# Kernel tuning notes

Measured on AMD Instinct MI355X. Metric: run time of the kernel, lower is better.

## Reference

```python
import jax, jax.numpy as jnp
import numpy as np

N = 8192
IN_DIM = 128
HID = 32


def setup_inputs() -> dict:
    key = jax.random.key(0)
    ks = jax.random.split(key, 8)
    x = jax.random.normal(ks[0], (N, IN_DIM), dtype=jnp.float32)
    adj = jax.random.uniform(ks[1], (N, N), dtype=jnp.float32)
    # Linear params (torch nn.Linear: y = x @ W.T + b); store as [in, out] for einsum.
    def lin(k, fan_in, fan_out):
        bound = 1.0 / np.sqrt(fan_in)
        kw, kb = jax.random.split(k)
        W = jax.random.uniform(kw, (fan_in, fan_out), minval=-bound, maxval=bound, dtype=jnp.float32)
        b = jax.random.uniform(kb, (fan_out,), minval=-bound, maxval=bound, dtype=jnp.float32)
        return W, b
    W1, b1 = lin(ks[2], IN_DIM, HID)
    W2, b2 = lin(ks[3], HID, HID)
    W3, b3 = lin(ks[4], HID, 1)
    return {"x": x, "adj": adj, "W1": W1, "b1": b1, "W2": W2, "b2": b2, "W3": W3, "b3": b3}


def reference(x, adj, W1, b1, W2, b2, W3, b3):
    # a_hat = adj + I (self loops)
    n = adj.shape[0]
    a_hat = adj + jnp.eye(n, dtype=adj.dtype)
    degree = jnp.sum(a_hat, axis=1)
    d_inv_sqrt = jnp.clip(degree, 1.0, None) ** -0.5  # [N]
    # D^-1/2 A D^-1/2 as row/col scaling (same math as diag matmuls, no O(N^3) waste)
    a_norm = d_inv_sqrt[:, None] * a_hat * d_inv_sqrt[None, :]
    h = jax.nn.relu(a_norm @ (x @ W1 + b1))
    h = jax.nn.relu(a_norm @ (h @ W2 + b2))
    logits = (h @ W3 + b3).squeeze(-1)  # [N]
    return logits
```

## Files before the change

### kernel.cpp

```cpp
#include <hip/hip_runtime.h>
#include <math.h>

#define N 8192
#define IN_DIM 128
#define HID 32

#define RB 128
#define KT 64
#define SK 8
#define KCHUNK (N / SK)

__device__ __forceinline__ void fma4(float4& acc, float a, const float4& b) {
    acc.x = fmaf(a, b.x, acc.x);
    acc.y = fmaf(a, b.y, acc.y);
    acc.z = fmaf(a, b.z, acc.z);
    acc.w = fmaf(a, b.w, acc.w);
}

__global__ __launch_bounds__(256) void k_degree(const float* __restrict__ adj,
                                                float* __restrict__ dinv) {
    int row = blockIdx.x;
    const float4* rp = (const float4*)(adj + (size_t)row * N);
    int t = threadIdx.x;
    float s = 0.f;
#pragma unroll
    for (int i = 0; i < 8; ++i) {
        float4 v = rp[t + i * 256];
        s += v.x + v.y + v.z + v.w;
    }
    for (int off = 32; off > 0; off >>= 1) s += __shfl_down(s, off, 64);
    __shared__ float red[4];
    if ((t & 63) == 0) red[t >> 6] = s;
    __syncthreads();
    if (t == 0) {
        float deg = red[0] + red[1] + red[2] + red[3] + 1.0f;
        deg = fmaxf(deg, 1.0f);
        dinv[row] = 1.0f / sqrtf(deg);
    }
}

__global__ __launch_bounds__(256) void k_z1(const float* __restrict__ x,
                                            const float* __restrict__ W1,
                                            const float* __restrict__ b1,
                                            const float* __restrict__ dinv,
                                            float* __restrict__ Zs) {
    __shared__ float Ws[IN_DIM * HID];
    __shared__ float xs[8 * IN_DIM];
    int t = threadIdx.x;
    int row0 = blockIdx.x * 8;
#pragma unroll
    for (int i = 0; i < 4; ++i)
        *(float4*)&Ws[(i * 256 + t) * 4] = *(const float4*)&W1[(i * 256 + t) * 4];
    *(float4*)&xs[t * 4] = *(const float4*)&x[(size_t)row0 * IN_DIM + t * 4];
    __syncthreads();
    int r = t >> 5, c = t & 31;
    float acc = b1[c];
#pragma unroll 8
    for (int k = 0; k < IN_DIM; ++k) acc = fmaf(xs[r * IN_DIM + k], Ws[k * HID + c], acc);
    int row = row0 + r;
    Zs[(size_t)row * HID + c] = dinv[row] * acc;
}

__global__ __launch_bounds__(256) void k_z2(const float* __restrict__ Hin,
                                            const float* __restrict__ W2,
                                            const float* __restrict__ b2,
                                            const float* __restrict__ dinv,
                                            float* __restrict__ Zs) {
    __shared__ float Ws[HID * HID];
    __shared__ float hs[8 * HID];
    int t = threadIdx.x;
    int row0 = blockIdx.x * 8;
    *(float4*)&Ws[t * 4] = *(const float4*)&W2[t * 4];
    if (t < 64) *(float4*)&hs[t * 4] = *(const float4*)&Hin[(size_t)row0 * HID + t * 4];
    __syncthreads();
    int r = t >> 5, c = t & 31;
    float acc = b2[c];
#pragma unroll
    for (int k = 0; k < HID; ++k) acc = fmaf(hs[r * HID + k], Ws[k * HID + c], acc);
    int row = row0 + r;
    Zs[(size_t)row * HID + c] = dinv[row] * acc;
}

__global__ __launch_bounds__(256) void k_spmm(const float* __restrict__ adj,
                                              const float* __restrict__ Zs,
                                              float* __restrict__ P) {
    __shared__ float As[RB][KT + 4];
    __shared__ float Bs[KT][HID];
    int t = threadIdx.x;
    int r0 = blockIdx.x * RB;
    int k0 = blockIdx.y * KCHUNK;
    int cg = t & 3;
    int rp2 = (t >> 2) * 2;
    float4 acc00 = {0, 0, 0, 0}, acc01 = {0, 0, 0, 0};
    float4 acc10 = {0, 0, 0, 0}, acc11 = {0, 0, 0, 0};

    for (int kt = k0; kt < k0 + KCHUNK; kt += KT) {
#pragma unroll
        for (int i = 0; i < 8; ++i) {
            int f = i * 256 + t;
            int row = f >> 4;
            int kc = (f & 15) << 2;
            *(float4*)&As[row][kc] = *(const float4*)&adj[(size_t)(r0 + row) * N + kt + kc];
        }
#pragma unroll
        for (int i = 0; i < 2; ++i) {
            int f = i * 256 + t;
            ((float4*)&Bs[0][0])[f] = ((const float4*)(Zs + (size_t)kt * HID))[f];
        }
        __syncthreads();
#pragma unroll
        for (int kk = 0; kk < KT; kk += 4) {
            float a0[4], a1[4];
            *(float4*)a0 = *(const float4*)&As[rp2][kk];
            *(float4*)a1 = *(const float4*)&As[rp2 + 1][kk];
#pragma unroll
            for (int j = 0; j < 4; ++j) {
                float4 z0 = *(const float4*)&Bs[kk + j][cg * 8];
                float4 z1 = *(const float4*)&Bs[kk + j][cg * 8 + 4];
                fma4(acc00, a0[j], z0);
                fma4(acc01, a0[j], z1);
                fma4(acc10, a1[j], z0);
                fma4(acc11, a1[j], z1);
            }
        }
        __syncthreads();
    }

    float* p0 = P + (size_t)(r0 + rp2) * HID + cg * 8;
    float* p1 = p0 + HID;
    atomicAdd(p0 + 0, acc00.x); atomicAdd(p0 + 1, acc00.y);
    atomicAdd(p0 + 2, acc00.z); atomicAdd(p0 + 3, acc00.w);
    atomicAdd(p0 + 4, acc01.x); atomicAdd(p0 + 5, acc01.y);
    atomicAdd(p0 + 6, acc01.z); atomicAdd(p0 + 7, acc01.w);
    atomicAdd(p1 + 0, acc10.x); atomicAdd(p1 + 1, acc10.y);
    atomicAdd(p1 + 2, acc10.z); atomicAdd(p1 + 3, acc10.w);
    atomicAdd(p1 + 4, acc11.x); atomicAdd(p1 + 5, acc11.y);
    atomicAdd(p1 + 6, acc11.z); atomicAdd(p1 + 7, acc11.w);
}

__global__ __launch_bounds__(256) void k_fin(const float* __restrict__ P,
                                             const float* __restrict__ Zs,
                                             const float* __restrict__ dinv,
                                             float* __restrict__ H) {
    int idx = blockIdx.x * 256 + threadIdx.x;
    int row = idx >> 5;
    float v = dinv[row] * (P[idx] + Zs[idx]);
    H[idx] = fmaxf(v, 0.f);
}

__global__ __launch_bounds__(256) void k_out(const float* __restrict__ H,
                                             const float* __restrict__ W3,
                                             const float* __restrict__ b3,
                                             float* __restrict__ out) {
    int i = blockIdx.x * 256 + threadIdx.x;
    const float4* hr = (const float4*)(H + (size_t)i * HID);
    const float4* w = (const float4*)W3;
    float acc = b3[0];
#pragma unroll
    for (int kk = 0; kk < 8; ++kk) {
        float4 h = hr[kk], ww = w[kk];
        acc += h.x * ww.x + h.y * ww.y + h.z * ww.z + h.w * ww.w;
    }
    out[i] = acc;
}

extern "C" void kernel_launch(void* const* d_in, const int* in_sizes, int n_in,
                              void* d_out, int out_size, void* d_ws, size_t ws_size,
                              hipStream_t stream) {
    const float* x   = (const float*)d_in[0];
    const float* adj = (const float*)d_in[1];
    const float* W1  = (const float*)d_in[2];
    const float* b1  = (const float*)d_in[3];
    const float* W2  = (const float*)d_in[4];
    const float* b2  = (const float*)d_in[5];
    const float* W3  = (const float*)d_in[6];
    const float* b3  = (const float*)d_in[7];
    float* out = (float*)d_out;

    float* dinv = (float*)d_ws;
    float* Zs   = dinv + N;
    float* P    = Zs + (size_t)N * HID;
    float* H    = P + (size_t)N * HID;

    k_degree<<<N, 256, 0, stream>>>(adj, dinv);
    k_z1<<<N / 8, 256, 0, stream>>>(x, W1, b1, dinv, Zs);

    hipMemsetAsync(P, 0, (size_t)N * HID * sizeof(float), stream);
    k_spmm<<<dim3(N / RB, SK), 256, 0, stream>>>(adj, Zs, P);
    k_fin<<<N * HID / 256, 256, 0, stream>>>(P, Zs, dinv, H);

    k_z2<<<N / 8, 256, 0, stream>>>(H, W2, b2, dinv, Zs);

    hipMemsetAsync(P, 0, (size_t)N * HID * sizeof(float), stream);
    k_spmm<<<dim3(N / RB, SK), 256, 0, stream>>>(adj, Zs, P);
    k_fin<<<N * HID / 256, 256, 0, stream>>>(P, Zs, dinv, H);

    k_out<<<N / 256, 256, 0, stream>>>(H, W3, b3, out);
}
```

Baseline: 611.9 us.

## Convert adjacency to fp16 once and use fdot2 SpMM with fused epilogue

The degree kernel now also writes an fp16 copy of the adjacency matrix. Both aggregation passes then stream that half-size copy instead of fp32. The SpMM is restructured: Z is stored transposed in fp16 and double-buffered in shared memory, each wave handles 4 rows across the full K range, and the inner product uses packed fp16 dot2 instructions. Split-K atomics, the memset and the separate finalize kernel are replaced by an in-block reduction that fuses the dinv scaling, self-loop add and ReLU. This cuts adjacency traffic for the two passes at the cost of one extra fp16 write and reduced precision.

Result: slower. 1.117 ms (+82.5%).

```diff
diff --git a/kernel.cpp b/kernel.cpp
--- a/kernel.cpp
+++ b/kernel.cpp
@@ -5,27 +5,46 @@
 #define IN_DIM 128
 #define HID 32
 
-#define RB 128
-#define KT 64
-#define SK 8
-#define KCHUNK (N / SK)
-
-__device__ __forceinline__ void fma4(float4& acc, float a, const float4& b) {
-    acc.x = fmaf(a, b.x, acc.x);
-    acc.y = fmaf(a, b.y, acc.y);
-    acc.z = fmaf(a, b.z, acc.z);
-    acc.w = fmaf(a, b.w, acc.w);
-}
-
-__global__ __launch_bounds__(256) void k_degree(const float* __restrict__ adj,
-                                                float* __restrict__ dinv) {
+#define WIN 512
+#define NWIN (N / WIN)
+#define BSTRIDE 520
+
+typedef _Float16 h2 __attribute__((ext_vector_type(2)));
+typedef _Float16 h4 __attribute__((ext_vector_type(4)));
+
+__device__ __forceinline__ h2 bch2(unsigned u) {
+    union { unsigned u; h2 h; } x; x.u = u; return x.h;
+}
+
+#if defined(__has_builtin)
+#if __has_builtin(__builtin_amdgcn_fdot2)
+#define HAVE_FDOT2 1
+#endif
+#endif
+
+__device__ __forceinline__ float dot2acc(h2 a, h2 b, float c) {
+#ifdef HAVE_FDOT2
+    return __builtin_amdgcn_fdot2(a, b, c, false);
+#else
+    return fmaf((float)a.x, (float)b.x, fmaf((float)a.y, (float)b.y, c));
+#endif
+}
+
+__global__ __launch_bounds__(256) void k_prep(const float* __restrict__ adj,
+                                              _Float16* __restrict__ adjh,
+                                              float* __restrict__ dinv) {
     int row = blockIdx.x;
+    int t = threadIdx.x;
     const float4* rp = (const float4*)(adj + (size_t)row * N);
-    int t = threadIdx.x;
+    h4* hp = (h4*)(adjh + (size_t)row * N);
     float s = 0.f;
 #pragma unroll
     for (int i = 0; i < 8; ++i) {
         float4 v = rp[t + i * 256];
+        h4 h;
+        h.x = (_Float16)v.x; h.y = (_Float16)v.y;
+        h.z = (_Float16)v.z; h.w = (_Float16)v.w;
+        hp[t + i * 256] = h;
         s += v.x + v.y + v.z + v.w;
     }
     for (int off = 32; off > 0; off >>= 1) s += __shfl_down(s, off, 64);
@@ -43,9 +62,11 @@
                                             const float* __restrict__ W1,
                                             const float* __restrict__ b1,
                                             const float* __restrict__ dinv,
-                                            float* __restrict__ Zs) {
+                                            float* __restrict__ Zs,
+                                            _Float16* __restrict__ Zt) {
     __shared__ float Ws[IN_DIM * HID];
     __shared__ float xs[8 * IN_DIM];
+    __shared__ float zt_t[8 * HID];
     int t = threadIdx.x;
     int row0 = blockIdx.x * 8;
 #pragma unroll
@@ -58,16 +79,27 @@
 #pragma unroll 8
     for (int k = 0; k < IN_DIM; ++k) acc = fmaf(xs[r * IN_DIM + k], Ws[k * HID + c], acc);
     int row = row0 + r;
-    Zs[(size_t)row * HID + c] = dinv[row] * acc;
+    float v = dinv[row] * acc;
+    Zs[(size_t)row * HID + c] = v;
+    zt_t[r * HID + c] = v;
+    __syncthreads();
+    if (t < HID) {
+        union { _Float16 h[8]; uint4 u; } pk;
+#pragma unroll
+        for (int rr = 0; rr < 8; ++rr) pk.h[rr] = (_Float16)zt_t[rr * HID + t];
+        *(uint4*)(Zt + (size_t)t * N + row0) = pk.u;
+    }
 }
 
 __global__ __launch_bounds__(256) void k_z2(const float* __restrict__ Hin,
                                             const float* __restrict__ W2,
                                             const float* __restrict__ b2,
                                             const float* __restrict__ dinv,
-                                            float* __restrict__ Zs) {
+                                            float* __restrict__ Zs,
+                                            _Float16* __restrict__ Zt) {
     __shared__ float Ws[HID * HID];
     __shared__ float hs[8 * HID];
+    __shared__ float zt_t[8 * HID];
     int t = threadIdx.x;
     int row0 = blockIdx.x * 8;
     *(float4*)&Ws[t * 4] = *(const float4*)&W2[t * 4];
@@ -78,74 +110,100 @@
 #pragma unroll
     for (int k = 0; k < HID; ++k) acc = fmaf(hs[r * HID + k], Ws[k * HID + c], acc);
     int row = row0 + r;
-    Zs[(size_t)row * HID + c] = dinv[row] * acc;
-}
-
-__global__ __launch_bounds__(256) void k_spmm(const float* __restrict__ adj,
-                                              const float* __restrict__ Zs,
-                                              float* __restrict__ P) {
-    __shared__ float As[RB][KT + 4];
-    __shared__ float Bs[KT][HID];
-    int t = threadIdx.x;
-    int r0 = blockIdx.x * RB;
-    int k0 = blockIdx.y * KCHUNK;
-    int cg = t & 3;
-    int rp2 = (t >> 2) * 2;
-    float4 acc00 = {0, 0, 0, 0}, acc01 = {0, 0, 0, 0};
-    float4 acc10 = {0, 0, 0, 0}, acc11 = {0, 0, 0, 0};
-
-    for (int kt = k0; kt < k0 + KCHUNK; kt += KT) {
-#pragma unroll
-        for (int i = 0; i < 8; ++i) {
-            int f = i * 256 + t;
-            int row = f >> 4;
-            int kc = (f & 15) << 2;
-            *(float4*)&As[row][kc] = *(const float4*)&adj[(size_t)(r0 + row) * N + kt + kc];
+    float v = dinv[row] * acc;
+    Zs[(size_t)row * HID + c] = v;
+    zt_t[r * HID + c] = v;
+    __syncthreads();
+    if (t < HID) {
+        union { _Float16 h[8]; uint4 u; } pk;
+#pragma unroll
+        for (int rr = 0; rr < 8; ++rr) pk.h[rr] = (_Float16)zt_t[rr * HID + t];
+        *(uint4*)(Zt + (size_t)t * N + row0) = pk.u;
+    }
+}
+
+__global__ __launch_bounds__(256, 2) void k_spmm(const _Float16* __restrict__ adjh,
+                                                 const _Float16* __restrict__ Ztg,
+                                                 const float* __restrict__ Zs,
+                                                 const float* __restrict__ dinv,
+                                                 float* __restrict__ H) {
+    __shared__ __align__(16) char smem[69632];
+    _Float16* zb = (_Float16*)smem;
+    float* scr = (float*)smem;
+
+    int t = threadIdx.x;
+    int wv = t >> 6, ln = t & 63;
+    int row0 = blockIdx.x * 16 + wv * 4;
+
+    float acc[4][32];
+#pragma unroll
+    for (int r = 0; r < 4; ++r)
+#pragma unroll
+        for (int c = 0; c < 32; ++c) acc[r][c] = 0.f;
+
+#pragma unroll
+    for (int i = 0; i < 8; ++i) {
+        int id = i * 256 + t;
+        int c = id >> 6;
+        int kk = (id & 63) * 8;
+        *(uint4*)(zb + c * BSTRIDE + kk) = *(const uint4*)(Ztg + (size_t)c * N + kk);
+    }
+    __syncthreads();
+
+    for (int w = 0; w < NWIN; ++w) {
+        if (w + 1 < NWIN) {
+            _Float16* dst = zb + ((w + 1) & 1) * 32 * BSTRIDE;
+#pragma unroll
+            for (int i = 0; i < 8; ++i) {
+                int id = i * 256 + t;
+                int c = id >> 6;
+                int kk = (id & 63) * 8;
+                *(uint4*)(dst + c * BSTRIDE + kk) =
+                    *(const uint4*)(Ztg + (size_t)c * N + (w + 1) * WIN + kk);
+            }
         }
-#pragma unroll
-        for (int i = 0; i < 2; ++i) {
-            int f = i * 256 + t;
-            ((float4*)&Bs[0][0])[f] = ((const float4*)(Zs + (size_t)kt * HID))[f];
-        }
-        __syncthreads();
-#pragma unroll
-        for (int kk = 0; kk < KT; kk += 4) {
-            float a0[4], a1[4];
-            *(float4*)a0 = *(const float4*)&As[rp2][kk];
-            *(float4*)a1 = *(const float4*)&As[rp2 + 1][kk];
-#pragma unroll
-            for (int j = 0; j < 4; ++j) {
-                float4 z0 = *(const float4*)&Bs[kk + j][cg * 8];
-                float4 z1 = *(const float4*)&Bs[kk + j][cg * 8 + 4];
-                fma4(acc00, a0[j], z0);
-                fma4(acc01, a0[j], z1);
-                fma4(acc10, a1[j], z0);
-                fma4(acc11, a1[j], z1);
+        const _Float16* B = zb + (w & 1) * 32 * BSTRIDE;
+
+        uint4 a[4];
+#pragma unroll
+        for (int r = 0; r < 4; ++r)
+            a[r] = *(const uint4*)(adjh + (size_t)(row0 + r) * N + w * WIN + ln * 8);
+
+#pragma unroll 8
+        for (int c = 0; c < 32; ++c) {
+            uint4 b = *(const uint4*)(B + c * BSTRIDE + ln * 8);
+            h2 b0 = bch2(b.x), b1 = bch2(b.y), b2 = bch2(b.z), b3 = bch2(b.w);
+#pragma unroll
+            for (int r = 0; r < 4; ++r) {
+                h2 a0 = bch2(a[r].x), a1 = bch2(a[r].y), a2 = bch2(a[r].z), a3 = bch2(a[r].w);
+                float s = acc[r][c];
+                s = dot2acc(a0, b0, s);
+                s = dot2acc(a1, b1, s);
+                s = dot2acc(a2, b2, s);
+                s = dot2acc(a3, b3, s);
+                acc[r][c] = s;
             }
         }
         __syncthreads();
     }
 
-    float* p0 = P + (size_t)(r0 + rp2) * HID + cg * 8;
-    float* p1 = p0 + HID;
-    atomicAdd(p0 + 0, acc00.x); atomicAdd(p0 + 1, acc00.y);
-    atomicAdd(p0 + 2, acc00.z); atomicAdd(p0 + 3, acc00.w);
-    atomicAdd(p0 + 4, acc01.x); atomicAdd(p0 + 5, acc01.y);
-    atomicAdd(p0 + 6, acc01.z); atomicAdd(p0 + 7, acc01.w);
-    atomicAdd(p1 + 0, acc10.x); atomicAdd(p1 + 1, acc10.y);
-    atomicAdd(p1 + 2, acc10.z); atomicAdd(p1 + 3, acc10.w);
-    atomicAdd(p1 + 4, acc11.x); atomicAdd(p1 + 5, acc11.y);
-    atomicAdd(p1 + 6, acc11.z); atomicAdd(p1 + 7, acc11.w);
-}
-
-__global__ __launch_bounds__(256) void k_fin(const float* __restrict__ P,
-                                             const float* __restrict__ Zs,
-                                             const float* __restrict__ dinv,
-                                             float* __restrict__ H) {
-    int idx = blockIdx.x * 256 + threadIdx.x;
-    int row = idx >> 5;
-    float v = dinv[row] * (P[idx] + Zs[idx]);
-    H[idx] = fmaxf(v, 0.f);
+    float* sw = scr + wv * (64 * 68);
+    for (int p = 0; p < 2; ++p) {
+#pragma unroll
+        for (int i = 0; i < 64; ++i) sw[i * 68 + ln] = acc[2 * p + (i >> 5)][i & 31];
+        __syncthreads();
+        float s = 0.f;
+#pragma unroll
+        for (int j = 0; j < 64; j += 4) {
+            float4 v = *(const float4*)(sw + ln * 68 + j);
+            s += v.x + v.y + v.z + v.w;
+        }
+        int row = row0 + 2 * p + (ln >> 5);
+        int col = ln & 31;
+        float val = dinv[row] * (s + Zs[(size_t)row * HID + col]);
+        H[(size_t)row * HID + col] = fmaxf(val, 0.f);
+        __syncthreads();
+    }
 }
 
 __global__ __launch_bounds__(256) void k_out(const float* __restrict__ H,
@@ -177,23 +235,17 @@
     const float* b3  = (const float*)d_in[7];
     float* out = (float*)d_out;
 
-    float* dinv = (float*)d_ws;
-    float* Zs   = dinv + N;
-    float* P    = Zs + (size_t)N * HID;
-    float* H    = P + (size_t)N * HID;
-
-    k_degree<<<N, 256, 0, stream>>>(adj, dinv);
-    k_z1<<<N / 8, 256, 0, stream>>>(x, W1, b1, dinv, Zs);
-
-    hipMemsetAsync(P, 0, (size_t)N * HID * sizeof(float), stream);
-    k_spmm<<<dim3(N / RB, SK), 256, 0, stream>>>(adj, Zs, P);
-    k_fin<<<N * HID / 256, 256, 0, stream>>>(P, Zs, dinv, H);
-
-    k_z2<<<N / 8, 256, 0, stream>>>(H, W2, b2, dinv, Zs);
-
-    hipMemsetAsync(P, 0, (size_t)N * HID * sizeof(float), stream);
-    k_spmm<<<dim3(N / RB, SK), 256, 0, stream>>>(adj, Zs, P);
-    k_fin<<<N * HID / 256, 256, 0, stream>>>(P, Zs, dinv, H);
-
+    char* ws = (char*)d_ws;
+    float* dinv   = (float*)ws;                       ws += 8192 * sizeof(float);
+    _Float16* adjh = (_Float16*)ws;                   ws += (size_t)N * N * sizeof(_Float16);
+    float* Zs     = (float*)ws;                       ws += (size_t)N * HID * sizeof(float);
+    _Float16* Zt  = (_Float16*)ws;                    ws += (size_t)N * HID * sizeof(_Float16);
+    float* H      = (float*)ws;
+
+    k_prep<<<N, 256, 0, stream>>>(adj, adjh, dinv);
+    k_z1<<<N / 8, 256, 0, stream>>>(x, W1, b1, dinv, Zs, Zt);
+    k_spmm<<<N / 16, 256, 0, stream>>>(adjh, Zt, Zs, dinv, H);
+    k_z2<<<N / 8, 256, 0, stream>>>(H, W2, b2, dinv, Zs, Zt);
+    k_spmm<<<N / 16, 256, 0, stream>>>(adjh, Zt, Zs, dinv, H);
     k_out<<<N / 256, 256, 0, stream>>>(H, W3, b3, out);
 }
```
